# Kernel tuning notes

Measured on AMD Instinct MI355X. Metric: run time of the kernel, lower is better.

The kernel has to match this reference:

```python
import jax, jax.numpy as jnp
import numpy as np

N_FEATURES = 1024
N_OUTPUTS = 512
N = 32768
N_DECISIONS = 3  # root + 2 internal nodes (depth-2 tree)
N_LEAVES = 4


def setup_inputs() -> dict:
    key = jax.random.key(0)
    k_x, k_dw, k_db, k_lw, k_lb = jax.random.split(key, 5)
    xs = jax.random.normal(k_x, (N, N_FEATURES), dtype=jnp.float32)
    # decision hyperplanes for nodes [root, left-child, right-child]
    dec_w = jax.random.normal(k_dw, (N_DECISIONS, N_FEATURES), dtype=jnp.float32) / np.sqrt(N_FEATURES)
    dec_b = jax.random.normal(k_db, (N_DECISIONS,), dtype=jnp.float32) * 0.01
    # linear leaves, ordered [LL, LR, RL, RR]
    leaf_w = jax.random.normal(k_lw, (N_LEAVES, N_FEATURES, N_OUTPUTS), dtype=jnp.float32) / np.sqrt(N_FEATURES)
    leaf_b = jax.random.normal(k_lb, (N_LEAVES, N_OUTPUTS), dtype=jnp.float32) * 0.01
    return {"xs": xs, "dec_w": dec_w, "dec_b": dec_b, "leaf_w": leaf_w, "leaf_b": leaf_b}


def reference(xs, dec_w, dec_b, leaf_w, leaf_b):
    # decisions at all 3 branch nodes: [N, 3] boolean (True -> go right)
    d = (xs @ dec_w.T + dec_b) > 0
    d0, d1, d2 = d[:, 0], d[:, 1], d[:, 2]
    # leaf index per sample: root False -> left subtree (node 1), True -> right subtree (node 2)
    leaf_idx = jnp.where(
        d0,
        jnp.where(d2, 3, 2),
        jnp.where(d1, 1, 0),
    )  # [N]
    # compute all leaf outputs densely (equivalent math to masked dispatch), then select
    outs = jnp.einsum("nf,kfd->nkd", xs, leaf_w) + leaf_b  # [N, 4, D]
    out = jnp.take_along_axis(outs, leaf_idx[:, None, None], axis=1)[:, 0]  # [N, D]
    return out
```

## Files before the change

kernel.cpp:

```cpp
#include <hip/hip_runtime.h>
#include <hip/hip_bf16.h>
#include <stdint.h>

#define NROWS 32768
#define NFEAT 1024
#define NOUT  512

typedef __attribute__((ext_vector_type(8))) short bf16x8;
typedef __attribute__((ext_vector_type(4))) short bf16x4;
typedef __attribute__((ext_vector_type(4))) float f32x4;

#define WS_CNT  0
#define WS_LIST 256
#define WS_BT   524544
#define WS_XB   (WS_BT + (size_t)4 * NOUT * NFEAT * 2)
#define WS_NEEDED (WS_XB + (size_t)NROWS * NFEAT * 2)

__global__ __launch_bounds__(256) void transpose_b_kernel(
    const float* __restrict__ lw, __hip_bfloat16* __restrict__ bt) {
  __shared__ float tile[32][33];
  int l = blockIdx.z;
  int k0 = blockIdx.x * 32;
  int d0 = blockIdx.y * 32;
  int x = threadIdx.x;
  int y = threadIdx.y;
  const float* src = lw + (size_t)l * NFEAT * NOUT;
#pragma unroll
  for (int i = 0; i < 4; ++i)
    tile[y * 4 + i][x] = src[(size_t)(k0 + y * 4 + i) * NOUT + d0 + x];
  __syncthreads();
  __hip_bfloat16* dst = bt + (size_t)l * NOUT * NFEAT;
#pragma unroll
  for (int i = 0; i < 4; ++i)
    dst[(size_t)(d0 + y * 4 + i) * NFEAT + k0 + x] = __float2bfloat16(tile[x][y * 4 + i]);
}

__global__ __launch_bounds__(256) void decide_kernel(
    const float* __restrict__ xs, const float* __restrict__ dw,
    const float* __restrict__ db, int* __restrict__ cnt, int* __restrict__ list,
    __hip_bfloat16* __restrict__ xsb ) {
  const int tid = threadIdx.x;
  const int lane = tid & 63;
  const int wv = tid >> 6;
  __shared__ int leaf_of[64];

  f32x4 w0[4], w1[4], w2[4];
#pragma unroll
  for (int c = 0; c < 4; ++c) {
    int idx = c * 256 + lane * 4;
    w0[c] = *(const f32x4*)(dw + idx);
    w1[c] = *(const f32x4*)(dw + NFEAT + idx);
    w2[c] = *(const f32x4*)(dw + 2 * NFEAT + idx);
  }
  float b0 = db[0], b1 = db[1], b2 = db[2];

  int rowbase = blockIdx.x * 64 + wv * 16;
  for (int r = 0; r < 16; ++r) {
    int row = rowbase + r;
    const float* xr = xs + (size_t)row * NFEAT;
    float s0 = 0.f, s1 = 0.f, s2 = 0.f;
#pragma unroll
    for (int c = 0; c < 4; ++c) {
      int idx = c * 256 + lane * 4;
      f32x4 xv = *(const f32x4*)(xr + idx);
#pragma unroll
      for (int j = 0; j < 4; ++j) {
        s0 += xv[j] * w0[c][j];
        s1 += xv[j] * w1[c][j];
        s2 += xv[j] * w2[c][j];
      }
      if (xsb) {
        union { bf16x4 v; __hip_bfloat16 h[4]; } pk;
#pragma unroll
        for (int j = 0; j < 4; ++j) pk.h[j] = __float2bfloat16(xv[j]);
        *(bf16x4*)(xsb + (size_t)row * NFEAT + idx) = pk.v;
      }
    }
#pragma unroll
    for (int off = 32; off > 0; off >>= 1) {
      s0 += __shfl_xor(s0, off);
      s1 += __shfl_xor(s1, off);
      s2 += __shfl_xor(s2, off);
    }
    if (lane == 0) {
      int lf = (s0 + b0 > 0.f) ? ((s2 + b2 > 0.f) ? 3 : 2)
                               : ((s1 + b1 > 0.f) ? 1 : 0);
      leaf_of[wv * 16 + r] = lf;
    }
  }
  __syncthreads();

  if (tid < 64) {
    int i = tid;
    int myleaf = leaf_of[i];
    int myrow = blockIdx.x * 64 + i;
    unsigned long long m0 = __ballot(myleaf == 0);
    unsigned long long m1 = __ballot(myleaf == 1);
    unsigned long long m2 = __ballot(myleaf == 2);
    unsigned long long m3 = __ballot(myleaf == 3);
    unsigned long long mym = (myleaf == 0) ? m0 : (myleaf == 1) ? m1
                           : (myleaf == 2) ? m2 : m3;
    unsigned long long below = (1ull << i) - 1ull;
    int rank = __popcll(mym & below);
    int base = 0;
    if (i < 4) {
      unsigned long long mi = (i == 0) ? m0 : (i == 1) ? m1 : (i == 2) ? m2 : m3;
      base = atomicAdd(&cnt[i], __popcll(mi));
    }
    int mybase = __shfl(base, myleaf);
    list[myleaf * NROWS + mybase + rank] = myrow;
  }
}

#define BM 128
#define BN 128
#define BK 64
#define KSTEPS (NFEAT / BK)

__device__ __forceinline__ bool decode_tile(const int* cnt, int& leaf, int& mloc,
                                            int& ntile, int& cc) {
  int bid = blockIdx.x;
  int cpx = (int)(gridDim.x >> 3);
  int swz = (bid & 7) * cpx + (bid >> 3);
  int mtile = swz >> 2;
  ntile = swz & 3;
  int c0 = cnt[0], c1 = cnt[1], c2 = cnt[2], c3 = cnt[3];
  int t0 = (c0 + BM - 1) / BM, t1 = (c1 + BM - 1) / BM;
  int t2 = (c2 + BM - 1) / BM, t3 = (c3 + BM - 1) / BM;
  if (mtile < t0)                     { leaf = 0; mloc = mtile;                cc = c0; }
  else if (mtile < t0 + t1)           { leaf = 1; mloc = mtile - t0;           cc = c1; }
  else if (mtile < t0 + t1 + t2)      { leaf = 2; mloc = mtile - t0 - t1;      cc = c2; }
  else if (mtile < t0 + t1 + t2 + t3) { leaf = 3; mloc = mtile - t0 - t1 - t2; cc = c3; }
  else return false;
  return true;
}

__global__ __launch_bounds__(256) void gemm_lds_kernel(
    const __hip_bfloat16* __restrict__ xsb, const __hip_bfloat16* __restrict__ bt,
    const float* __restrict__ lb, const int* __restrict__ cnt,
    const int* __restrict__ list, float* __restrict__ out) {
  __shared__ __hip_bfloat16 Al[BM * BK];
  __shared__ __hip_bfloat16 Bl[BN * BK];
  __shared__ int rows_s[BM];

  int leaf, mloc, ntile, cc;
  if (!decode_tile(cnt, leaf, mloc, ntile, cc)) return;

  const int tid = threadIdx.x;
  if (tid < BM) {
    int i = mloc * BM + tid;
    rows_s[tid] = (i < cc) ? list[leaf * NROWS + i] : -1;
  }
  __syncthreads();

  const int lane = tid & 63;
  const int wv = tid >> 6;
  const int g8 = (((lane & 7) ^ (lane >> 3)) << 3);
  const __hip_bfloat16* asrc[4];
  const __hip_bfloat16* bsrc[4];
#pragma unroll
  for (int j = 0; j < 4; ++j) {
    int tr = wv * 32 + j * 8 + (lane >> 3);
    int grow = rows_s[tr];
    if (grow < 0) grow = 0;
    asrc[j] = xsb + (size_t)grow * NFEAT + g8;
    bsrc[j] = bt + ((size_t)leaf * NOUT + ntile * BN + tr) * NFEAT + g8;
  }

  const int wr = (wv >> 1) * 64;
  const int wc = (wv & 1) * 64;
  f32x4 acc[4][4];
#pragma unroll
  for (int m = 0; m < 4; ++m)
#pragma unroll
    for (int n = 0; n < 4; ++n) acc[m][n] = (f32x4){0.f, 0.f, 0.f, 0.f};

  for (int ks = 0; ks < KSTEPS; ++ks) {
    if (ks) __syncthreads();
#pragma unroll
    for (int j = 0; j < 4; ++j) {
      __builtin_amdgcn_global_load_lds(
          (const __attribute__((address_space(1))) void*)(asrc[j] + ks * BK),
          (__attribute__((address_space(3))) void*)(&Al[(wv * 4 + j) * 512]),
          16, 0, 0);
      __builtin_amdgcn_global_load_lds(
          (const __attribute__((address_space(1))) void*)(bsrc[j] + ks * BK),
          (__attribute__((address_space(3))) void*)(&Bl[(wv * 4 + j) * 512]),
          16, 0, 0);
    }
    __syncthreads();

#pragma unroll
    for (int kk = 0; kk < 2; ++kk) {
      bf16x8 af[4], bfr[4];
      int gk = kk * 4 + (lane >> 4);
#pragma unroll
      for (int m = 0; m < 4; ++m) {
        int r = wr + m * 16 + (lane & 15);
        af[m] = *(const bf16x8*)(&Al[r * BK + ((gk ^ (r & 7)) << 3)]);
      }
#pragma unroll
      for (int n = 0; n < 4; ++n) {
        int r = wc + n * 16 + (lane & 15);
        bfr[n] = *(const bf16x8*)(&Bl[r * BK + ((gk ^ (r & 7)) << 3)]);
      }
#pragma unroll
      for (int m = 0; m < 4; ++m)
#pragma unroll
        for (int n = 0; n < 4; ++n)
          acc[m][n] = __builtin_amdgcn_mfma_f32_16x16x32_bf16(
              af[m], bfr[n], acc[m][n], 0, 0, 0);
    }
  }

  int colb = ntile * BN + wc;
#pragma unroll
  for (int n = 0; n < 4; ++n) {
    int col = colb + n * 16 + (lane & 15);
    float bias = lb[leaf * NOUT + col];
#pragma unroll
    for (int m = 0; m < 4; ++m) {
#pragma unroll
      for (int r = 0; r < 4; ++r) {
        int lrow = wr + m * 16 + (lane >> 4) * 4 + r;
        int grow = rows_s[lrow];
        if (grow >= 0) out[(size_t)grow * NOUT + col] = acc[m][n][r] + bias;
      }
    }
  }
}

__global__ __launch_bounds__(256) void gemm_fallback_kernel(
    const float* __restrict__ xs, const __hip_bfloat16* __restrict__ bt,
    const float* __restrict__ lb, const int* __restrict__ cnt,
    const int* __restrict__ list, float* __restrict__ out) {
  __shared__ __hip_bfloat16 Al[BM * BK];
  __shared__ __hip_bfloat16 Bl[BN * BK];
  __shared__ int rows_s[BM];

  int leaf, mloc, ntile, cc;
  if (!decode_tile(cnt, leaf, mloc, ntile, cc)) return;

  const int tid = threadIdx.x;
  if (tid < BM) {
    int i = mloc * BM + tid;
    rows_s[tid] = (i < cc) ? list[leaf * NROWS + i] : -1;
  }
  __syncthreads();

  const int srow = tid >> 1;
  const int shalf = tid & 1;
  int a_grow = rows_s[srow];
  int a_clamp = (a_grow < 0) ? 0 : a_grow;
  const float* aptr = xs + (size_t)a_clamp * NFEAT + shalf * 32;
  const __hip_bfloat16* bptr =
      bt + ((size_t)leaf * NOUT + ntile * BN + srow) * NFEAT + shalf * 32;

  const int lane = tid & 63;
  const int wv = tid >> 6;
  const int wr = (wv >> 1) * 64;
  const int wc = (wv & 1) * 64;

  f32x4 acc[4][4];
#pragma unroll
  for (int m = 0; m < 4; ++m)
#pragma unroll
    for (int n = 0; n < 4; ++n) acc[m][n] = (f32x4){0.f, 0.f, 0.f, 0.f};

  f32x4 av[8];
  bf16x8 bv[4];
#define LOAD_TILE(K0)                                                        \
  {                                                                          \
    _Pragma("unroll") for (int j = 0; j < 8; ++j)                            \
        av[j] = *(const f32x4*)(aptr + (K0) + j * 4);                        \
    _Pragma("unroll") for (int j = 0; j < 4; ++j)                            \
        bv[j] = *(const bf16x8*)(bptr + (K0) + j * 8);                       \
  }

  LOAD_TILE(0);

  for (int ks = 0; ks < KSTEPS; ++ks) {
#pragma unroll
    for (int j = 0; j < 4; ++j) {
      union { bf16x8 v; __hip_bfloat16 h[8]; } pk;
#pragma unroll
      for (int e = 0; e < 8; ++e)
        pk.h[e] = __float2bfloat16(av[j * 2 + (e >> 2)][e & 3]);
      int g = shalf * 4 + j;
      *(bf16x8*)(&Al[srow * BK + ((g ^ (srow & 7)) << 3)]) = pk.v;
    }
#pragma unroll
    for (int j = 0; j < 4; ++j) {
      int g = shalf * 4 + j;
      *(bf16x8*)(&Bl[srow * BK + ((g ^ (srow & 7)) << 3)]) = bv[j];
    }
    __syncthreads();

    if (ks + 1 < KSTEPS) LOAD_TILE((ks + 1) * BK);

#pragma unroll
    for (int kk = 0; kk < 2; ++kk) {
      bf16x8 af[4], bfr[4];
      int gk = kk * 4 + (lane >> 4);
#pragma unroll
      for (int m = 0; m < 4; ++m) {
        int r = wr + m * 16 + (lane & 15);
        af[m] = *(const bf16x8*)(&Al[r * BK + ((gk ^ (r & 7)) << 3)]);
      }
#pragma unroll
      for (int n = 0; n < 4; ++n) {
        int r = wc + n * 16 + (lane & 15);
        bfr[n] = *(const bf16x8*)(&Bl[r * BK + ((gk ^ (r & 7)) << 3)]);
      }
#pragma unroll
      for (int m = 0; m < 4; ++m)
#pragma unroll
        for (int n = 0; n < 4; ++n)
          acc[m][n] = __builtin_amdgcn_mfma_f32_16x16x32_bf16(
              af[m], bfr[n], acc[m][n], 0, 0, 0);
    }
    __syncthreads();
  }

  int colb = ntile * BN + wc;
#pragma unroll
  for (int n = 0; n < 4; ++n) {
    int col = colb + n * 16 + (lane & 15);
    float bias = lb[leaf * NOUT + col];
#pragma unroll
    for (int m = 0; m < 4; ++m) {
#pragma unroll
      for (int r = 0; r < 4; ++r) {
        int lrow = wr + m * 16 + (lane >> 4) * 4 + r;
        int grow = rows_s[lrow];
        if (grow >= 0) out[(size_t)grow * NOUT + col] = acc[m][n][r] + bias;
      }
    }
  }
}

extern "C" void kernel_launch(void* const* d_in, const int* in_sizes, int n_in,
                              void* d_out, int out_size, void* d_ws, size_t ws_size,
                              hipStream_t stream) {
  const float* xs = (const float*)d_in[0];
  const float* dw = (const float*)d_in[1];
  const float* db = (const float*)d_in[2];
  const float* lw = (const float*)d_in[3];
  const float* lb = (const float*)d_in[4];
  float* out = (float*)d_out;
  char* ws = (char*)d_ws;
  int* cnt = (int*)(ws + WS_CNT);
  int* list = (int*)(ws + WS_LIST);
  __hip_bfloat16* bt = (__hip_bfloat16*)(ws + WS_BT);
  bool big = ws_size >= WS_NEEDED;
  __hip_bfloat16* xsb = big ? (__hip_bfloat16*)(ws + WS_XB) : nullptr;

  hipMemsetAsync(cnt, 0, 4 * sizeof(int), stream);
  transpose_b_kernel<<<dim3(32, 16, 4), dim3(32, 8), 0, stream>>>(lw, bt);
  decide_kernel<<<512, 256, 0, stream>>>(xs, dw, db, cnt, list, xsb);
  if (big)
    gemm_lds_kernel<<<1040, 256, 0, stream>>>(xsb, bt, lb, cnt, list, out);
  else
    gemm_fallback_kernel<<<1040, 256, 0, stream>>>(xs, bt, lb, cnt, list, out);
}
```

Baseline: 128.6 us.

## Fuse weight transpose into decide kernel and widen per-lane loads

Merges the leaf-weight transpose/bf16 conversion kernel into the decision kernel as extra blocks, so both memory-bound phases share one launch and can overlap. It also halves the rows per decide block to double the block count, widens per-lane loads to 8 floats with 16-byte bf16 stores, and replaces the memset with a tiny zeroing kernel. The cost is a more complex fused kernel with branching block roles and partially idle wavefronts in the compaction step.

```diff
diff --git a/kernel.cpp b/kernel.cpp
--- a/kernel.cpp
+++ b/kernel.cpp
@@ -7,7 +7,6 @@
 #define NOUT  512
 
 typedef __attribute__((ext_vector_type(8))) short bf16x8;
-typedef __attribute__((ext_vector_type(4))) short bf16x4;
 typedef __attribute__((ext_vector_type(4))) float f32x4;
 
 #define WS_CNT  0
@@ -16,64 +15,87 @@
 #define WS_XB   (WS_BT + (size_t)4 * NOUT * NFEAT * 2)
 #define WS_NEEDED (WS_XB + (size_t)NROWS * NFEAT * 2)
 
-__global__ __launch_bounds__(256) void transpose_b_kernel(
-    const float* __restrict__ lw, __hip_bfloat16* __restrict__ bt) {
-  __shared__ float tile[32][33];
-  int l = blockIdx.z;
-  int k0 = blockIdx.x * 32;
-  int d0 = blockIdx.y * 32;
-  int x = threadIdx.x;
-  int y = threadIdx.y;
-  const float* src = lw + (size_t)l * NFEAT * NOUT;
-#pragma unroll
-  for (int i = 0; i < 4; ++i)
-    tile[y * 4 + i][x] = src[(size_t)(k0 + y * 4 + i) * NOUT + d0 + x];
-  __syncthreads();
-  __hip_bfloat16* dst = bt + (size_t)l * NOUT * NFEAT;
-#pragma unroll
-  for (int i = 0; i < 4; ++i)
-    dst[(size_t)(d0 + y * 4 + i) * NFEAT + k0 + x] = __float2bfloat16(tile[x][y * 4 + i]);
-}
-
-__global__ __launch_bounds__(256) void decide_kernel(
+#define NDEC_BLOCKS 1024
+#define NTR_BLOCKS  512
+
+__global__ __launch_bounds__(64) void zero_cnt_kernel(int* __restrict__ cnt) {
+  if (threadIdx.x < 4) cnt[threadIdx.x] = 0;
+}
+
+__global__ __launch_bounds__(256) void decide_tr_kernel(
     const float* __restrict__ xs, const float* __restrict__ dw,
-    const float* __restrict__ db, int* __restrict__ cnt, int* __restrict__ list,
-    __hip_bfloat16* __restrict__ xsb ) {
+    const float* __restrict__ db, const float* __restrict__ lw,
+    __hip_bfloat16* __restrict__ bt, int* __restrict__ cnt,
+    int* __restrict__ list, __hip_bfloat16* __restrict__ xsb ) {
+  __shared__ float smem[32 * 33];
   const int tid = threadIdx.x;
+  int b = blockIdx.x;
+
+  if (b >= NDEC_BLOCKS) {
+    int tb = b - NDEC_BLOCKS;
+    int l = tb >> 7;
+    int t = tb & 127;
+    int d0 = (t >> 3) * 32;
+    int k00 = (t & 7) * 128;
+    int x = tid & 31, y = tid >> 5;
+    const float* src = lw + (size_t)l * NFEAT * NOUT;
+    __hip_bfloat16* dst = bt + (size_t)l * NOUT * NFEAT;
+    float (*tile)[33] = (float(*)[33])smem;
+    for (int kk = 0; kk < 4; ++kk) {
+      int k0 = k00 + kk * 32;
+#pragma unroll
+      for (int i = 0; i < 4; ++i)
+        tile[y * 4 + i][x] = src[(size_t)(k0 + y * 4 + i) * NOUT + d0 + x];
+      __syncthreads();
+#pragma unroll
+      for (int i = 0; i < 4; ++i)
+        dst[(size_t)(d0 + y * 4 + i) * NFEAT + k0 + x] =
+            __float2bfloat16(tile[x][y * 4 + i]);
+      __syncthreads();
+    }
+    return;
+  }
+
+  int* leaf_of = (int*)smem;
   const int lane = tid & 63;
   const int wv = tid >> 6;
-  __shared__ int leaf_of[64];
 
   f32x4 w0[4], w1[4], w2[4];
 #pragma unroll
-  for (int c = 0; c < 4; ++c) {
-    int idx = c * 256 + lane * 4;
-    w0[c] = *(const f32x4*)(dw + idx);
-    w1[c] = *(const f32x4*)(dw + NFEAT + idx);
-    w2[c] = *(const f32x4*)(dw + 2 * NFEAT + idx);
-  }
+  for (int c = 0; c < 2; ++c)
+#pragma unroll
+    for (int h = 0; h < 2; ++h) {
+      int idx = c * 512 + lane * 8 + h * 4;
+      w0[c * 2 + h] = *(const f32x4*)(dw + idx);
+      w1[c * 2 + h] = *(const f32x4*)(dw + NFEAT + idx);
+      w2[c * 2 + h] = *(const f32x4*)(dw + 2 * NFEAT + idx);
+    }
   float b0 = db[0], b1 = db[1], b2 = db[2];
 
-  int rowbase = blockIdx.x * 64 + wv * 16;
-  for (int r = 0; r < 16; ++r) {
+  int rowbase = b * 32 + wv * 8;
+  for (int r = 0; r < 8; ++r) {
     int row = rowbase + r;
     const float* xr = xs + (size_t)row * NFEAT;
     float s0 = 0.f, s1 = 0.f, s2 = 0.f;
 #pragma unroll
-    for (int c = 0; c < 4; ++c) {
-      int idx = c * 256 + lane * 4;
-      f32x4 xv = *(const f32x4*)(xr + idx);
+    for (int c = 0; c < 2; ++c) {
+      int idx = c * 512 + lane * 8;
+      f32x4 xv0 = *(const f32x4*)(xr + idx);
+      f32x4 xv1 = *(const f32x4*)(xr + idx + 4);
 #pragma unroll
       for (int j = 0; j < 4; ++j) {
-        s0 += xv[j] * w0[c][j];
-        s1 += xv[j] * w1[c][j];
-        s2 += xv[j] * w2[c][j];
+        s0 += xv0[j] * w0[c * 2][j] + xv1[j] * w0[c * 2 + 1][j];
+        s1 += xv0[j] * w1[c * 2][j] + xv1[j] * w1[c * 2 + 1][j];
+        s2 += xv0[j] * w2[c * 2][j] + xv1[j] * w2[c * 2 + 1][j];
       }
       if (xsb) {
-        union { bf16x4 v; __hip_bfloat16 h[4]; } pk;
-#pragma unroll
-        for (int j = 0; j < 4; ++j) pk.h[j] = __float2bfloat16(xv[j]);
-        *(bf16x4*)(xsb + (size_t)row * NFEAT + idx) = pk.v;
+        union { bf16x8 v; __hip_bfloat16 h[8]; } pk;
+#pragma unroll
+        for (int j = 0; j < 4; ++j) {
+          pk.h[j] = __float2bfloat16(xv0[j]);
+          pk.h[j + 4] = __float2bfloat16(xv1[j]);
+        }
+        *(bf16x8*)(xsb + (size_t)row * NFEAT + idx) = pk.v;
       }
     }
 #pragma unroll
@@ -85,21 +107,21 @@
     if (lane == 0) {
       int lf = (s0 + b0 > 0.f) ? ((s2 + b2 > 0.f) ? 3 : 2)
                                : ((s1 + b1 > 0.f) ? 1 : 0);
-      leaf_of[wv * 16 + r] = lf;
+      leaf_of[wv * 8 + r] = lf;
     }
   }
   __syncthreads();
 
   if (tid < 64) {
     int i = tid;
-    int myleaf = leaf_of[i];
-    int myrow = blockIdx.x * 64 + i;
+    int myleaf = (i < 32) ? leaf_of[i] : -1;
+    int myrow = b * 32 + i;
     unsigned long long m0 = __ballot(myleaf == 0);
     unsigned long long m1 = __ballot(myleaf == 1);
     unsigned long long m2 = __ballot(myleaf == 2);
     unsigned long long m3 = __ballot(myleaf == 3);
     unsigned long long mym = (myleaf == 0) ? m0 : (myleaf == 1) ? m1
-                           : (myleaf == 2) ? m2 : m3;
+                           : (myleaf == 2) ? m2 : (myleaf == 3) ? m3 : 0ull;
     unsigned long long below = (1ull << i) - 1ull;
     int rank = __popcll(mym & below);
     int base = 0;
@@ -107,8 +129,8 @@
       unsigned long long mi = (i == 0) ? m0 : (i == 1) ? m1 : (i == 2) ? m2 : m3;
       base = atomicAdd(&cnt[i], __popcll(mi));
     }
-    int mybase = __shfl(base, myleaf);
-    list[myleaf * NROWS + mybase + rank] = myrow;
+    int mybase = __shfl(base, (myleaf < 0) ? 0 : myleaf);
+    if (i < 32) list[myleaf * NROWS + mybase + rank] = myrow;
   }
 }
 
@@ -355,9 +377,9 @@
   bool big = ws_size >= WS_NEEDED;
   __hip_bfloat16* xsb = big ? (__hip_bfloat16*)(ws + WS_XB) : nullptr;
 
-  hipMemsetAsync(cnt, 0, 4 * sizeof(int), stream);
-  transpose_b_kernel<<<dim3(32, 16, 4), dim3(32, 8), 0, stream>>>(lw, bt);
-  decide_kernel<<<512, 256, 0, stream>>>(xs, dw, db, cnt, list, xsb);
+  zero_cnt_kernel<<<1, 64, 0, stream>>>(cnt);
+  decide_tr_kernel<<<NDEC_BLOCKS + NTR_BLOCKS, 256, 0, stream>>>(
+      xs, dw, db, lw, bt, cnt, list, xsb);
   if (big)
     gemm_lds_kernel<<<1040, 256, 0, stream>>>(xsb, bt, lb, cnt, list, out);
   else
```

New measurement: 105.9 us. 1.21x faster.
